# Optimization experiments

Measured on AMD Instinct MI355X. Metric: run time of the kernel, lower is better.

## Reference

```python
import jax, jax.numpy as jnp
from jax import lax
import numpy as np

B, N, K, H = 8, 4096, 24, 32  # graphs, nodes/graph, kNN k, hidden_dim


def setup_inputs() -> dict:
    key = jax.random.key(0)
    ks = jax.random.split(key, 16)
    W = lambda k, i, o: jax.random.normal(k, (i, o), jnp.float32) * 0.1
    b = lambda k, o: jax.random.normal(k, (o,), jnp.float32) * 0.01
    inp = {
        'x_lc': jax.random.normal(ks[0], (B * N, 4), jnp.float32),
        'batch_lc': jnp.repeat(jnp.arange(B, dtype=jnp.int64), N),
        'enc_w1': W(ks[1], 4, H), 'enc_b1': b(ks[2], H),
        'enc_w2': W(ks[3], H, H), 'enc_b2': b(ks[4], H),
        'conv1_w': W(ks[5], 2 * H, H), 'conv1_b': b(ks[6], H),
        'conv2_w': W(ks[7], 2 * H, H), 'conv2_b': b(ks[8], H),
        'conv3_w': W(ks[9], 2 * H, H), 'conv3_b': b(ks[10], H),
        'out_w1': W(ks[11], H, 32), 'out_b1': b(ks[12], 32),
        'out_w2': W(ks[13], 32, 16), 'out_b2': b(ks[14], 16),
        'out_w3': W(ks[15], 16, 8), 'out_b3': jnp.zeros((8,), jnp.float32),
    }
    return inp


def _dynamic_edge_conv(x, w, bias):
    # x: [B, N, D]; kNN within each graph, edge msg nn([x_i, x_j - x_i]), max-agg
    d2 = jnp.sum(x * x, axis=-1)  # [B, N]
    dist = d2[:, :, None] + d2[:, None, :] - 2.0 * jnp.einsum('bnd,bmd->bnm', x, x)
    # kNN index computation is non-differentiable (as in PyG knn)
    idx = lax.top_k(-lax.stop_gradient(dist), K)[1]  # [B, N, K], includes self
    xj = jax.vmap(lambda xb, ib: xb[ib])(x, idx)  # [B, N, K, D]
    xi = jnp.broadcast_to(x[:, :, None, :], xj.shape)
    e = jnp.concatenate([xi, xj - xi], axis=-1)  # [B, N, K, 2D]
    h = jax.nn.elu(e @ w + bias)  # [B, N, K, H]
    return jnp.max(h, axis=2)  # [B, N, H]


def reference(x_lc, batch_lc, enc_w1, enc_b1, enc_w2, enc_b2,
              conv1_w, conv1_b, conv2_w, conv2_b, conv3_w, conv3_b,
              out_w1, out_b1, out_w2, out_b2, out_w3, out_b3):
    # lc_encode
    h = jax.nn.elu(x_lc @ enc_w1 + enc_b1)
    h = jax.nn.elu(h @ enc_w2 + enc_b2)  # [B*N, H]
    h = h.reshape(B, N, H)  # equal-sized sorted graphs
    h = _dynamic_edge_conv(h, conv1_w, conv1_b)
    h = _dynamic_edge_conv(h, conv2_w, conv2_b)
    h = _dynamic_edge_conv(h, conv3_w, conv3_b)
    h = h.reshape(B * N, H)
    o = jax.nn.elu(h @ out_w1 + out_b1)
    o = jax.nn.elu(o @ out_w2 + out_b2)
    o = o @ out_w3 + out_b3  # [B*N, 8]
    return (o, batch_lc)
```

## Files before the change

### kernel.cpp

```cpp
#include <hip/hip_runtime.h>
#include <cstddef>
#include <cstdint>

#define BN    32768
#define NG    4096
#define KNN   24
#define KPW   14
#define KM    32
#define CHK   128
#define NBQ   64
#define STKD  16
#define TRIG  13

typedef float f32x4_t __attribute__((ext_vector_type(4)));
typedef short s16x8_t __attribute__((ext_vector_type(8)));

__device__ __forceinline__ float elu_f(float x) {
    return x > 0.f ? x : expm1f(x);
}

__device__ __forceinline__ unsigned short f2bf(float f) {
    unsigned u = __float_as_uint(f);
    unsigned r = (u + 0x7FFFu + ((u >> 16) & 1u)) >> 16;
    return (unsigned short)r;
}

__device__ __forceinline__ void gload_lds16(const void* g, void* l) {
    __builtin_amdgcn_global_load_lds(
        (const __attribute__((address_space(1))) unsigned*)g,
        (__attribute__((address_space(3))) unsigned*)l, 16, 0, 0);
}

__device__ __forceinline__ void pack_node(int n, const float* hv,
    unsigned short* __restrict__ hbf, unsigned short* __restrict__ til,
    float* __restrict__ d2b)
{
    __align__(16) unsigned short us[32];
    float s = 0.f;
#pragma unroll
    for (int k = 0; k < 32; ++k) {
        us[k] = f2bf(hv[k]);
        float v = __uint_as_float(((unsigned)us[k]) << 16);
        s = fmaf(v, v, s);
    }
    d2b[n] = s;
    const uint4* up = reinterpret_cast<const uint4*>(us);
    uint4* lp = reinterpret_cast<uint4*>(hbf + (size_t)n * 32);
#pragma unroll
    for (int j = 0; j < 4; ++j) lp[j] = up[j];
    const int g = n >> 12, ln = n & 4095, tile = ln >> 4, c = ln & 15;
    unsigned short* tb = til + (size_t)g * 131072 + tile * 512 + c * 8;
#pragma unroll
    for (int kg = 0; kg < 4; ++kg)
        *reinterpret_cast<uint4*>(tb + kg * 128) = up[kg];
}

__global__ __launch_bounds__(128) void k_encoder(
    const float* __restrict__ x,
    const float* __restrict__ w1, const float* __restrict__ b1,
    const float* __restrict__ w2, const float* __restrict__ b2,
    float* __restrict__ hOut, float* __restrict__ d2Out,
    unsigned short* __restrict__ hbf, unsigned short* __restrict__ til,
    float* __restrict__ d2b)
{
    __shared__ float sw1[4 * 32];
    __shared__ float sb1[32];
    __shared__ float sw2[32 * 32];
    __shared__ float sb2[32];
    int tid = threadIdx.x;
    sw1[tid] = w1[tid];
    if (tid < 32) sb1[tid] = b1[tid];
    for (int i = tid; i < 1024; i += 128) sw2[i] = w2[i];
    if (tid >= 32 && tid < 64) sb2[tid - 32] = b2[tid - 32];
    __syncthreads();

    int node = blockIdx.x * 128 + tid;
    float4 xv = reinterpret_cast<const float4*>(x)[node];

    float h1[32];
#pragma unroll
    for (int o = 0; o < 32; ++o) {
        float s = sb1[o];
        s = fmaf(xv.x, sw1[o], s);
        s = fmaf(xv.y, sw1[32 + o], s);
        s = fmaf(xv.z, sw1[64 + o], s);
        s = fmaf(xv.w, sw1[96 + o], s);
        h1[o] = elu_f(s);
    }
    float h2[32];
    float d2 = 0.f;
#pragma unroll
    for (int o = 0; o < 32; ++o) {
        float s = sb2[o];
#pragma unroll
        for (int f = 0; f < 32; ++f) s = fmaf(h1[f], sw2[f * 32 + o], s);
        float v = elu_f(s);
        h2[o] = v;
        d2 = fmaf(v, v, d2);
    }
    float4* hp = reinterpret_cast<float4*>(hOut) + (size_t)node * 8;
#pragma unroll
    for (int j = 0; j < 8; ++j)
        hp[j] = make_float4(h2[4 * j], h2[4 * j + 1], h2[4 * j + 2], h2[4 * j + 3]);
    d2Out[node] = d2;
    pack_node(node, h2, hbf, til, d2b);
}

#define CHAIN14(nk_) do { \
    unsigned nk = (nk_); \
    _Pragma("unroll") \
    for (int jj = 0; jj < KPW; ++jj) { \
        unsigned tj = top[jj]; \
        unsigned lo = nk < tj ? nk : tj; \
        unsigned hi = nk < tj ? tj : nk; \
        top[jj] = lo; nk = hi; \
    } \
} while (0)

__global__ __launch_bounds__(512, 4) void k_knn(
    const unsigned short* __restrict__ til,
    const unsigned short* __restrict__ hbf,
    const float* __restrict__ d2b,
    const float* __restrict__ hf,
    const float* __restrict__ d2x,
    int* __restrict__ idxOut,
    const float* __restrict__ cw, const float* __restrict__ cb,
    float* __restrict__ Abuf, float* __restrict__ Bbuf)
{
    __shared__ __align__(16) unsigned char smem[49152];
    constexpr int SD2 = 0;
    constexpr int STK = 16384;
    constexpr int LST = 16384;
    constexpr int SW  = 0;
    constexpr int SH  = 8192;
    constexpr int MG  = 30720;
    constexpr int DSV = 38912;
    constexpr int SB  = 47104;

    const int tid = threadIdx.x;
    const int lane = tid & 63;
    const int wid = __builtin_amdgcn_readfirstlane(tid >> 6);
    const int qt = wid >> 1;
    const int par = wid & 1;
    const int bid = blockIdx.x;
    const int g = bid >> 6;
    const int gbase = g << 12;
    const int blockq = (bid & 63) * NBQ;
    const int qnode = gbase + blockq + qt * 16 + (lane & 15);
    const int rg = (lane >> 4) * 4;

    gload_lds16(d2b + gbase + wid * 256 + lane * 4, smem + SD2 + wid * 1024);
    gload_lds16(d2b + gbase + 2048 + wid * 256 + lane * 4,
                smem + SD2 + 8192 + wid * 1024);

    s16x8_t bfrag = *reinterpret_cast<const s16x8_t*>(
        hbf + (size_t)qnode * 32 + (lane >> 4) * 8);
    const float qd2 = d2b[qnode];
    const float nqd2h = -0.5f * qd2;

    unsigned top[KPW];
#pragma unroll
    for (int j = 0; j < KPW; ++j) top[j] = 0xFFFFFFFFu;
    unsigned thresh = 0xFFFFFFFFu;
    int pcnt = 0;

    const char* gtw = (const char*)til + (size_t)g * 262144
                    + (size_t)par * 1024 + (size_t)lane * 16;
    const float* d2s = reinterpret_cast<const float*>(smem + SD2);
    unsigned* stkl = reinterpret_cast<unsigned*>(smem + STK + wid * 4096) + lane;

    __syncthreads();

    s16x8_t af[4];
#pragma unroll
    for (int i = 0; i < 4; ++i)
        af[i] = *reinterpret_cast<const s16x8_t*>(gtw + i * 2048);

    for (int c = 0; c < 32; ++c) {
        s16x8_t an[4];
        if (c < 31) {
#pragma unroll
            for (int i = 0; i < 4; ++i)
                an[i] = *reinterpret_cast<const s16x8_t*>(
                    gtw + (size_t)(c + 1) * 8192 + i * 2048);
        } else {
#pragma unroll
            for (int i = 0; i < 4; ++i) an[i] = af[i];
        }
        f32x4_t cv[4];
#pragma unroll
        for (int i = 0; i < 4; ++i)
            cv[i] = *reinterpret_cast<const f32x4_t*>(
                d2s + c * 128 + (i * 2 + par) * 16 + rg);
#pragma unroll
        for (int i = 0; i < 4; ++i) {
            const int t = i * 2 + par;
            f32x4_t acc;
#pragma unroll
            for (int r = 0; r < 4; ++r) acc[r] = fmaf(-0.5f, cv[i][r], nqd2h);
            acc = __builtin_amdgcn_mfma_f32_16x16x32_bf16(af[i], bfrag, acc, 0, 0, 0);
            const int cid0 = c * CHK + t * 16 + rg;
#pragma unroll
            for (int r = 0; r < 4; ++r) {
                unsigned key = (__float_as_uint(acc[r]) & 0xFFFFF000u)
                             | (unsigned)(cid0 + r);
                stkl[pcnt * 64] = key;
                pcnt += (key < thresh) ? 1 : 0;
            }
            if (__any(pcnt >= TRIG)) {
#pragma unroll 1
                for (int j = 0; j < STKD; ++j) {
                    if (!__any(pcnt > j)) break;
                    unsigned kk = stkl[j * 64];
                    unsigned k = (j < pcnt) ? kk : 0xFFFFFFFFu;
                    CHAIN14(k);
                }
                pcnt = 0;
                thresh = top[KPW - 1];
            }
        }
#pragma unroll
        for (int i = 0; i < 4; ++i) af[i] = an[i];
    }
#pragma unroll 1
    for (int j = 0; j < STKD; ++j) {
        if (!__any(pcnt > j)) break;
        unsigned kk = stkl[j * 64];
        unsigned k = (j < pcnt) ? kk : 0xFFFFFFFFu;
        CHAIN14(k);
    }
    __syncthreads();

    unsigned* lst = reinterpret_cast<unsigned*>(smem + LST);
#pragma unroll
    for (int j = 0; j < KPW; ++j) lst[(wid * 64 + lane) * KPW + j] = top[j];
    __syncthreads();

    int* mg = reinterpret_cast<int*>(smem + MG);
    float* dstv = reinterpret_cast<float*>(smem + DSV);

    if (tid < NBQ) {
        const int q = tid;
        unsigned mt[KM];
#pragma unroll
        for (int j = 0; j < KM; ++j) mt[j] = 0xFFFFFFFFu;
        for (int li = 0; li < 8; ++li) {
            const unsigned* lk = lst +
                (((q >> 4) * 2 + (li >> 2)) * 64 + (li & 3) * 16 + (q & 15)) * KPW;
            for (int j = 0; j < KPW; ++j) {
                unsigned key = lk[j];
                if (key >= mt[KM - 1]) break;
                unsigned nk = key;
#pragma unroll
                for (int jj = 0; jj < KM; ++jj) {
                    unsigned tj = mt[jj];
                    unsigned lo = nk < tj ? nk : tj;
                    unsigned hi = nk < tj ? tj : nk;
                    mt[jj] = lo; nk = hi;
                }
            }
        }
#pragma unroll
        for (int s = 0; s < KM; ++s) mg[q * 32 + s] = (int)(mt[s] & 0xFFFu);
    }
    __syncthreads();

    float* sw = reinterpret_cast<float*>(smem + SW);
    float* sh = reinterpret_cast<float*>(smem + SH);
    float* sb = reinterpret_cast<float*>(smem + SB);
    for (int i = tid; i < 2048; i += 512) sw[i] = cw[i];
    for (int i = tid; i < 2048; i += 512)
        sh[i] = hf[(size_t)(gbase + blockq) * 32 + i];
    if (tid < 32) sb[tid] = cb[tid];

    {
        const int q = tid >> 3;
        const int s0 = tid & 7;
        const int qn = gbase + blockq + q;
        const float4* qp = reinterpret_cast<const float4*>(hf) + (size_t)qn * 8;
        float4 qf[8];
#pragma unroll
        for (int j = 0; j < 8; ++j) qf[j] = qp[j];
        const float qd2e = d2x[qn];
#pragma unroll
        for (int ss = 0; ss < 4; ++ss) {
            const int s = s0 + ss * 8;
            const int cid = mg[q * 32 + s];
            const int cn = gbase + cid;
            const float4* cp = reinterpret_cast<const float4*>(hf) + (size_t)cn * 8;
            float ax = 0.f, ay = 0.f, az = 0.f, aw = 0.f;
#pragma unroll
            for (int jj = 0; jj < 8; ++jj) {
                float4 cc = cp[jj];
                ax = fmaf(qf[jj].x, cc.x, ax);
                ay = fmaf(qf[jj].y, cc.y, ay);
                az = fmaf(qf[jj].z, cc.z, az);
                aw = fmaf(qf[jj].w, cc.w, aw);
            }
            float dot = (ax + ay) + (az + aw);
            dstv[q * 32 + s] = fmaf(-2.f, dot, qd2e + d2x[cn]);
        }
    }
    __syncthreads();

    if (tid < NBQ) {
        const int q = tid;
        float bd[KNN]; int bi[KNN];
#pragma unroll
        for (int j = 0; j < KNN; ++j) { bd[j] = 1e30f; bi[j] = 0; }
        for (int s = 0; s < KM; ++s) {
            float nd = dstv[q * 32 + s];
            int ni = mg[q * 32 + s];
            if (nd < bd[KNN - 1]) {
#pragma unroll
                for (int jj = 0; jj < KNN; ++jj) {
                    bool lt = nd < bd[jj];
                    float td = bd[jj]; int ti = bi[jj];
                    bd[jj] = lt ? nd : td;
                    bi[jj] = lt ? ni : ti;
                    nd = lt ? td : nd;
                    ni = lt ? ti : ni;
                }
            }
        }
        int* o = idxOut + (size_t)(gbase + blockq + q) * KNN;
#pragma unroll
        for (int j = 0; j < KNN; ++j) o[j] = bi[j];
    }

    {
        const int n = tid >> 3;
        const int o0 = (tid & 7) * 4;
        const float* hr = sh + n * 32;
        const int node = gbase + blockq + n;
        float hreg[32];
#pragma unroll
        for (int j = 0; j < 8; ++j) {
            float4 v = *reinterpret_cast<const float4*>(hr + j * 4);
            hreg[4 * j] = v.x; hreg[4 * j + 1] = v.y;
            hreg[4 * j + 2] = v.z; hreg[4 * j + 3] = v.w;
        }
        float4 s1 = make_float4(0.f, 0.f, 0.f, 0.f);
        float4 s2 = make_float4(0.f, 0.f, 0.f, 0.f);
#pragma unroll
        for (int f = 0; f < 32; ++f) {
            float hv = hreg[f];
            float4 wa = *reinterpret_cast<const float4*>(sw + f * 32 + o0);
            float4 wb = *reinterpret_cast<const float4*>(sw + (32 + f) * 32 + o0);
            s1.x = fmaf(hv, wa.x, s1.x); s1.y = fmaf(hv, wa.y, s1.y);
            s1.z = fmaf(hv, wa.z, s1.z); s1.w = fmaf(hv, wa.w, s1.w);
            s2.x = fmaf(hv, wb.x, s2.x); s2.y = fmaf(hv, wb.y, s2.y);
            s2.z = fmaf(hv, wb.z, s2.z); s2.w = fmaf(hv, wb.w, s2.w);
        }
        float4 bv = *reinterpret_cast<const float4*>(sb + o0);
        float4 av = make_float4(s1.x - s2.x + bv.x, s1.y - s2.y + bv.y,
                                s1.z - s2.z + bv.z, s1.w - s2.w + bv.w);
        *reinterpret_cast<float4*>(Abuf + (size_t)node * 32 + o0) = av;
        *reinterpret_cast<float4*>(Bbuf + (size_t)node * 32 + o0) = s2;
    }
}

template <bool LAST>
__global__ __launch_bounds__(128) void k_aggregate(
    const float* __restrict__ A, const float* __restrict__ Bv,
    const int* __restrict__ idx,
    float* __restrict__ hOut, float* __restrict__ d2Out,
    unsigned short* __restrict__ hbf, unsigned short* __restrict__ til,
    float* __restrict__ d2b,
    const float* __restrict__ w1, const float* __restrict__ b1,
    const float* __restrict__ w2, const float* __restrict__ b2,
    const float* __restrict__ w3, const float* __restrict__ b3,
    float* __restrict__ out)
{
    __shared__ float sw1[1024];
    __shared__ float sb1[32];
    __shared__ float sw2[512];
    __shared__ float sb2[16];
    __shared__ float sw3[128];
    __shared__ float sb3[8];
    int tid = threadIdx.x;
    if (LAST) {
        for (int i = tid; i < 1024; i += 128) sw1[i] = w1[i];
        for (int i = tid; i < 512; i += 128) sw2[i] = w2[i];
        sw3[tid] = w3[tid];
        if (tid < 32) sb1[tid] = b1[tid];
        if (tid >= 32 && tid < 48) sb2[tid - 32] = b2[tid - 32];
        if (tid >= 48 && tid < 56) sb3[tid - 48] = b3[tid - 48];
        __syncthreads();
    }

    int node = blockIdx.x * 128 + tid;
    int g = node >> 12;
    const int* ip = idx + (size_t)node * KNN;

    float4 m[8];
#pragma unroll
    for (int j = 0; j < 8; ++j) m[j] = make_float4(-1e30f, -1e30f, -1e30f, -1e30f);

    for (int k = 0; k < KNN; ++k) {
        int cand = (g << 12) + ip[k];
        const float4* bp = reinterpret_cast<const float4*>(Bv) + (size_t)cand * 8;
#pragma unroll
        for (int j = 0; j < 8; ++j) {
            float4 b = bp[j];
            m[j].x = fmaxf(m[j].x, b.x);
            m[j].y = fmaxf(m[j].y, b.y);
            m[j].z = fmaxf(m[j].z, b.z);
            m[j].w = fmaxf(m[j].w, b.w);
        }
    }
    const float4* ap = reinterpret_cast<const float4*>(A) + (size_t)node * 8;
    float hv[32];
    float d2 = 0.f;
#pragma unroll
    for (int j = 0; j < 8; ++j) {
        float4 a = ap[j];
        float4 v;
        v.x = elu_f(a.x + m[j].x);
        v.y = elu_f(a.y + m[j].y);
        v.z = elu_f(a.z + m[j].z);
        v.w = elu_f(a.w + m[j].w);
        d2 = fmaf(v.x, v.x, d2);
        d2 = fmaf(v.y, v.y, d2);
        d2 = fmaf(v.z, v.z, d2);
        d2 = fmaf(v.w, v.w, d2);
        hv[4 * j] = v.x; hv[4 * j + 1] = v.y; hv[4 * j + 2] = v.z; hv[4 * j + 3] = v.w;
    }

    if (!LAST) {
        float4* hp = reinterpret_cast<float4*>(hOut) + (size_t)node * 8;
#pragma unroll
        for (int j = 0; j < 8; ++j)
            hp[j] = make_float4(hv[4 * j], hv[4 * j + 1], hv[4 * j + 2], hv[4 * j + 3]);
        d2Out[node] = d2;
        pack_node(node, hv, hbf, til, d2b);
    } else {
        float o1[32];
#pragma unroll
        for (int o = 0; o < 32; ++o) {
            float s = sb1[o];
#pragma unroll
            for (int f = 0; f < 32; ++f) s = fmaf(hv[f], sw1[f * 32 + o], s);
            o1[o] = elu_f(s);
        }
        float o2[16];
#pragma unroll
        for (int o = 0; o < 16; ++o) {
            float s = sb2[o];
#pragma unroll
            for (int f = 0; f < 32; ++f) s = fmaf(o1[f], sw2[f * 16 + o], s);
            o2[o] = elu_f(s);
        }
        float o3[8];
#pragma unroll
        for (int o = 0; o < 8; ++o) {
            float s = sb3[o];
#pragma unroll
            for (int f = 0; f < 16; ++f) s = fmaf(o2[f], sw3[f * 8 + o], s);
            o3[o] = s;
        }
        float4* op = reinterpret_cast<float4*>(out) + (size_t)node * 2;
        op[0] = make_float4(o3[0], o3[1], o3[2], o3[3]);
        op[1] = make_float4(o3[4], o3[5], o3[6], o3[7]);
        out[(size_t)BN * 8 + node] = (float)(node >> 12);
    }
}

extern "C" void kernel_launch(void* const* d_in, const int* in_sizes, int n_in,
                              void* d_out, int out_size, void* d_ws, size_t ws_size,
                              hipStream_t stream)
{
    (void)in_sizes; (void)n_in; (void)out_size; (void)ws_size;
    const float* x      = (const float*)d_in[0];
    const float* enc_w1 = (const float*)d_in[2];
    const float* enc_b1 = (const float*)d_in[3];
    const float* enc_w2 = (const float*)d_in[4];
    const float* enc_b2 = (const float*)d_in[5];
    const float* conv_w[3] = { (const float*)d_in[6], (const float*)d_in[8], (const float*)d_in[10] };
    const float* conv_b[3] = { (const float*)d_in[7], (const float*)d_in[9], (const float*)d_in[11] };
    const float* out_w1 = (const float*)d_in[12];
    const float* out_b1 = (const float*)d_in[13];
    const float* out_w2 = (const float*)d_in[14];
    const float* out_b2 = (const float*)d_in[15];
    const float* out_w3 = (const float*)d_in[16];
    const float* out_b3 = (const float*)d_in[17];

    char* ws = (char*)d_ws;
    float*          hA   = (float*)(ws + 0);
    float*          hB   = (float*)(ws + 4194304);
    unsigned short* hbfA = (unsigned short*)(ws + 8388608);
    unsigned short* hbfB = (unsigned short*)(ws + 10485760);
    unsigned short* tilA = (unsigned short*)(ws + 12582912);
    unsigned short* tilB = (unsigned short*)(ws + 14680064);
    float*          d2A  = (float*)(ws + 16777216);
    float*          d2B  = (float*)(ws + 16908288);
    float*          d2bA = (float*)(ws + 17039360);
    float*          d2bB = (float*)(ws + 17170432);
    int*            idx  = (int*)(ws + 17301504);
    float*          Abuf = (float*)(ws + 20447232);
    float*          Bbuf = (float*)(ws + 24641536);

    k_encoder<<<256, 128, 0, stream>>>(x, enc_w1, enc_b1, enc_w2, enc_b2,
                                       hA, d2A, hbfA, tilA, d2bA);

    float* hin = hA;   float* d2in = d2A;   float* d2bin = d2bA;
    unsigned short* hbfin = hbfA; unsigned short* tilin = tilA;
    float* hout = hB;  float* d2out = d2B;  float* d2bout = d2bB;
    unsigned short* hbfout = hbfB; unsigned short* tilout = tilB;

    for (int l = 0; l < 3; ++l) {
        k_knn<<<512, 512, 0, stream>>>(tilin, hbfin, d2bin, hin, d2in, idx,
                                       conv_w[l], conv_b[l], Abuf, Bbuf);
        if (l < 2) {
            k_aggregate<false><<<256, 128, 0, stream>>>(
                Abuf, Bbuf, idx, hout, d2out, hbfout, tilout, d2bout,
                nullptr, nullptr, nullptr, nullptr, nullptr, nullptr, nullptr);
        } else {
            k_aggregate<true><<<256, 128, 0, stream>>>(
                Abuf, Bbuf, idx, nullptr, nullptr, nullptr, nullptr, nullptr,
                out_w1, out_b1, out_w2, out_b2, out_w3, out_b3, (float*)d_out);
        }
        float* tf; unsigned short* ts;
        tf = hin; hin = hout; hout = tf;
        tf = d2in; d2in = d2out; d2out = tf;
        tf = d2bin; d2bin = d2bout; d2bout = tf;
        ts = hbfin; hbfin = hbfout; hbfout = ts;
        ts = tilin; tilin = tilout; tilout = ts;
    }
}
```

Before: 589.6 us.

## Split kNN kernel into candidate scan and parallel refine kernels

The fused kNN kernel is split into k_scan, which writes the 32 bf16-screened candidate ids per query to a scratch buffer (reusing tilout), and k_refine, a 128-thread kernel over 16 queries per block that recomputes exact fp32 distances and the per-node linear projections. The serial 64-thread insertion sort for the top-24 is replaced by a parallel rank computation across 8 threads per query. The tail of the heavy scan kernel no longer runs the refinement phase with most of its 512 threads idle, and the refinement work is spread over more, smaller blocks. The cost is an extra launch and a global round trip for the candidate list.

Measured after the change: 587.2 us. Within noise of the previous version (-0.4%).

```diff
diff --git a/kernel.cpp b/kernel.cpp
--- a/kernel.cpp
+++ b/kernel.cpp
@@ -117,25 +117,16 @@
     } \
 } while (0)
 
-__global__ __launch_bounds__(512, 4) void k_knn(
+__global__ __launch_bounds__(512, 4) void k_scan(
     const unsigned short* __restrict__ til,
     const unsigned short* __restrict__ hbf,
     const float* __restrict__ d2b,
-    const float* __restrict__ hf,
-    const float* __restrict__ d2x,
-    int* __restrict__ idxOut,
-    const float* __restrict__ cw, const float* __restrict__ cb,
-    float* __restrict__ Abuf, float* __restrict__ Bbuf)
+    unsigned short* __restrict__ mgs)
 {
     __shared__ __align__(16) unsigned char smem[49152];
     constexpr int SD2 = 0;
     constexpr int STK = 16384;
     constexpr int LST = 16384;
-    constexpr int SW  = 0;
-    constexpr int SH  = 8192;
-    constexpr int MG  = 30720;
-    constexpr int DSV = 38912;
-    constexpr int SB  = 47104;
 
     const int tid = threadIdx.x;
     const int lane = tid & 63;
@@ -236,10 +227,9 @@
     for (int j = 0; j < KPW; ++j) lst[(wid * 64 + lane) * KPW + j] = top[j];
     __syncthreads();
 
-    int* mg = reinterpret_cast<int*>(smem + MG);
-    float* dstv = reinterpret_cast<float*>(smem + DSV);
-
-    if (tid < NBQ) {
+    if (wid != 0) return;
+
+    {
         const int q = tid;
         unsigned mt[KM];
 #pragma unroll
@@ -260,83 +250,98 @@
                 }
             }
         }
-#pragma unroll
-        for (int s = 0; s < KM; ++s) mg[q * 32 + s] = (int)(mt[s] & 0xFFFu);
-    }
+        unsigned short* mrow = mgs + (size_t)(gbase + blockq + q) * 32;
+#pragma unroll
+        for (int s = 0; s < KM; ++s)
+            mrow[s] = (unsigned short)(mt[s] & 0xFFFu);
+    }
+}
+
+__global__ __launch_bounds__(128) void k_refine(
+    const unsigned short* __restrict__ mgs,
+    const float* __restrict__ hf,
+    const float* __restrict__ d2x,
+    const float* __restrict__ cw, const float* __restrict__ cb,
+    int* __restrict__ idxOut,
+    float* __restrict__ Abuf, float* __restrict__ Bbuf)
+{
+    __shared__ float sw[2048];
+    __shared__ float sb[32];
+    __shared__ __align__(16) float dstv[16][36];
+    __shared__ int mgl[16][32];
+
+    const int tid = threadIdx.x;
+    const int bid = blockIdx.x;
+    const int g = bid >> 8;
+    const int gbase = g << 12;
+    const int blockq = (bid & 255) * 16;
+
+    for (int i = tid; i < 2048; i += 128) sw[i] = cw[i];
+    if (tid < 32) sb[tid] = cb[tid];
+    for (int i = tid; i < 512; i += 128)
+        mgl[i >> 5][i & 31] =
+            (int)mgs[(size_t)(gbase + blockq + (i >> 5)) * 32 + (i & 31)];
     __syncthreads();
 
-    float* sw = reinterpret_cast<float*>(smem + SW);
-    float* sh = reinterpret_cast<float*>(smem + SH);
-    float* sb = reinterpret_cast<float*>(smem + SB);
-    for (int i = tid; i < 2048; i += 512) sw[i] = cw[i];
-    for (int i = tid; i < 2048; i += 512)
-        sh[i] = hf[(size_t)(gbase + blockq) * 32 + i];
-    if (tid < 32) sb[tid] = cb[tid];
+    const int q  = tid >> 3;
+    const int s0 = tid & 7;
+    const int qn = gbase + blockq + q;
+
+    const float4* qp = reinterpret_cast<const float4*>(hf) + (size_t)qn * 8;
+    float4 qf[8];
+#pragma unroll
+    for (int j = 0; j < 8; ++j) qf[j] = qp[j];
+    const float qd2e = d2x[qn];
+    int cids[4];
+#pragma unroll
+    for (int ss = 0; ss < 4; ++ss) {
+        const int s = s0 + ss * 8;
+        const int cid = mgl[q][s];
+        cids[ss] = cid;
+        const int cn = gbase + cid;
+        const float4* cp = reinterpret_cast<const float4*>(hf) + (size_t)cn * 8;
+        float ax = 0.f, ay = 0.f, az = 0.f, aw = 0.f;
+#pragma unroll
+        for (int jj = 0; jj < 8; ++jj) {
+            float4 cc = cp[jj];
+            ax = fmaf(qf[jj].x, cc.x, ax);
+            ay = fmaf(qf[jj].y, cc.y, ay);
+            az = fmaf(qf[jj].z, cc.z, az);
+            aw = fmaf(qf[jj].w, cc.w, aw);
+        }
+        float dot = (ax + ay) + (az + aw);
+        dstv[q][s] = fmaf(-2.f, dot, qd2e + d2x[cn]);
+    }
+    __syncthreads();
 
     {
-        const int q = tid >> 3;
-        const int s0 = tid & 7;
-        const int qn = gbase + blockq + q;
-        const float4* qp = reinterpret_cast<const float4*>(hf) + (size_t)qn * 8;
-        float4 qf[8];
-#pragma unroll
-        for (int j = 0; j < 8; ++j) qf[j] = qp[j];
-        const float qd2e = d2x[qn];
+        float dsr[32];
+        const float4* dvp = reinterpret_cast<const float4*>(dstv[q]);
+#pragma unroll
+        for (int jj = 0; jj < 8; ++jj) {
+            float4 t = dvp[jj];
+            dsr[4 * jj] = t.x; dsr[4 * jj + 1] = t.y;
+            dsr[4 * jj + 2] = t.z; dsr[4 * jj + 3] = t.w;
+        }
+        int* o = idxOut + (size_t)qn * KNN;
 #pragma unroll
         for (int ss = 0; ss < 4; ++ss) {
             const int s = s0 + ss * 8;
-            const int cid = mg[q * 32 + s];
-            const int cn = gbase + cid;
-            const float4* cp = reinterpret_cast<const float4*>(hf) + (size_t)cn * 8;
-            float ax = 0.f, ay = 0.f, az = 0.f, aw = 0.f;
-#pragma unroll
-            for (int jj = 0; jj < 8; ++jj) {
-                float4 cc = cp[jj];
-                ax = fmaf(qf[jj].x, cc.x, ax);
-                ay = fmaf(qf[jj].y, cc.y, ay);
-                az = fmaf(qf[jj].z, cc.z, az);
-                aw = fmaf(qf[jj].w, cc.w, aw);
-            }
-            float dot = (ax + ay) + (az + aw);
-            dstv[q * 32 + s] = fmaf(-2.f, dot, qd2e + d2x[cn]);
-        }
-    }
-    __syncthreads();
-
-    if (tid < NBQ) {
-        const int q = tid;
-        float bd[KNN]; int bi[KNN];
-#pragma unroll
-        for (int j = 0; j < KNN; ++j) { bd[j] = 1e30f; bi[j] = 0; }
-        for (int s = 0; s < KM; ++s) {
-            float nd = dstv[q * 32 + s];
-            int ni = mg[q * 32 + s];
-            if (nd < bd[KNN - 1]) {
-#pragma unroll
-                for (int jj = 0; jj < KNN; ++jj) {
-                    bool lt = nd < bd[jj];
-                    float td = bd[jj]; int ti = bi[jj];
-                    bd[jj] = lt ? nd : td;
-                    bi[jj] = lt ? ni : ti;
-                    nd = lt ? td : nd;
-                    ni = lt ? ti : ni;
-                }
-            }
-        }
-        int* o = idxOut + (size_t)(gbase + blockq + q) * KNN;
-#pragma unroll
-        for (int j = 0; j < KNN; ++j) o[j] = bi[j];
+            const float di = dsr[s];
+            int rank = 0;
+#pragma unroll
+            for (int j = 0; j < 32; ++j)
+                rank += (dsr[j] < di || (dsr[j] == di && j < s)) ? 1 : 0;
+            if (rank < KNN) o[rank] = cids[ss];
+        }
     }
 
     {
-        const int n = tid >> 3;
-        const int o0 = (tid & 7) * 4;
-        const float* hr = sh + n * 32;
-        const int node = gbase + blockq + n;
+        const int o0 = s0 * 4;
         float hreg[32];
 #pragma unroll
         for (int j = 0; j < 8; ++j) {
-            float4 v = *reinterpret_cast<const float4*>(hr + j * 4);
+            float4 v = qp[j];
             hreg[4 * j] = v.x; hreg[4 * j + 1] = v.y;
             hreg[4 * j + 2] = v.z; hreg[4 * j + 3] = v.w;
         }
@@ -355,8 +360,8 @@
         float4 bv = *reinterpret_cast<const float4*>(sb + o0);
         float4 av = make_float4(s1.x - s2.x + bv.x, s1.y - s2.y + bv.y,
                                 s1.z - s2.z + bv.z, s1.w - s2.w + bv.w);
-        *reinterpret_cast<float4*>(Abuf + (size_t)node * 32 + o0) = av;
-        *reinterpret_cast<float4*>(Bbuf + (size_t)node * 32 + o0) = s2;
+        *reinterpret_cast<float4*>(Abuf + (size_t)qn * 32 + o0) = av;
+        *reinterpret_cast<float4*>(Bbuf + (size_t)qn * 32 + o0) = s2;
     }
 }
 
@@ -509,8 +514,10 @@
     unsigned short* hbfout = hbfB; unsigned short* tilout = tilB;
 
     for (int l = 0; l < 3; ++l) {
-        k_knn<<<512, 512, 0, stream>>>(tilin, hbfin, d2bin, hin, d2in, idx,
-                                       conv_w[l], conv_b[l], Abuf, Bbuf);
+        unsigned short* mgs = tilout;
+        k_scan<<<512, 512, 0, stream>>>(tilin, hbfin, d2bin, mgs);
+        k_refine<<<2048, 128, 0, stream>>>(mgs, hin, d2in,
+                                           conv_w[l], conv_b[l], idx, Abuf, Bbuf);
         if (l < 2) {
             k_aggregate<false><<<256, 128, 0, stream>>>(
                 Abuf, Bbuf, idx, hout, d2out, hbfout, tilout, d2bout,
```
